# Optimization experiments

Hardware: AMD Instinct MI355X
Metric: run time of the kernel (lower is better)

The kernel has to match this reference:

```python
import jax, jax.numpy as jnp
import numpy as np

K_MASK = -2.3819763e+38
B, T, D, N, K, H = 2, 4096, 2048, 8, 1, 256


def apply_rope(inputs, positions, head_dim):
    # inputs: [B, T, n, H], positions: [B, T]
    fraction = 2.0 * jnp.arange(0, head_dim // 2, dtype=jnp.float32) / head_dim
    timescale = 10000.0 ** fraction  # [H/2]
    sinusoid_inp = positions[..., None].astype(jnp.float32) / timescale  # [B,T,H/2]
    sinusoid_inp = sinusoid_inp[..., None, :]  # [B,T,1,H/2]
    sin, cos = jnp.sin(sinusoid_inp), jnp.cos(sinusoid_inp)
    first_half, second_half = jnp.split(inputs, 2, axis=-1)
    first_part = first_half * cos - second_half * sin
    second_part = second_half * cos + first_half * sin
    return jnp.concatenate([first_part, second_part], axis=-1).astype(inputs.dtype)


def setup_inputs() -> dict:
    key = jax.random.key(0)
    kx, kq, kkv, ko = jax.random.split(key, 4)
    x = jax.random.normal(kx, (B, T, D), dtype=jnp.float32)
    segment_pos = jnp.broadcast_to(jnp.arange(T, dtype=jnp.int32), (B, T))
    attn_mask = jnp.broadcast_to(
        jnp.tril(jnp.ones((T, T), dtype=bool)), (B, T, T))  # causal
    q_w = jax.random.normal(kq, (N, D, H), dtype=jnp.float32) * 0.02
    kv_w = jax.random.normal(kkv, (2, K, D, H), dtype=jnp.float32) * 0.02
    out_w = jax.random.normal(ko, (N, H, D), dtype=jnp.float32) * 0.02
    return {"x": x, "segment_pos": segment_pos, "attn_mask": attn_mask,
            "q_w": q_w, "kv_w": kv_w, "out_w": out_w}


def reference(x, segment_pos, attn_mask, q_w, kv_w, out_w):
    # Projections (GQA branch: num_kv_heads != num_heads)
    query_proj = jnp.einsum('btd,ndh->btnh', x, q_w)          # [B,T,N,H]
    kv_proj = jnp.einsum('bsd,ckdh->cbskh', x, kv_w)          # [2,B,T,K,H]
    key_proj, value_proj = kv_proj[0], kv_proj[1]

    query_proj = apply_rope(query_proj, segment_pos, head_dim=H)
    query_scaled = query_proj * H ** (-0.5)
    key_proj = apply_rope(key_proj, segment_pos, head_dim=H)

    # Repeat KV heads for GQA (num_kv_heads == 1 -> N heads)
    value_proj = jnp.repeat(value_proj, N, axis=-2)           # [B,S,N,H]
    key_proj = jnp.repeat(key_proj, N, axis=-2)               # [B,S,N,H]

    logits = jnp.einsum('btnh,bsnh->btns', query_scaled, key_proj)
    padded_logits = jnp.where(attn_mask[:, :, None, :], logits, K_MASK)
    probs = jax.nn.softmax(padded_logits, axis=-1).astype(key_proj.dtype)
    encoded = jnp.einsum('btns,bsnh->btnh', probs, value_proj)
    attn_output = jnp.einsum('btnh,nhd->btd', encoded, out_w)
    return attn_output
```

## Files before the change

kernel.cpp:

```cpp
#include <hip/hip_runtime.h>

#define T_SEQ 4096
#define D_MODEL 2048
#define N_HEADS 8
#define HDIM 256

typedef unsigned int uint32;
typedef unsigned short u16;
typedef __attribute__((ext_vector_type(8))) short short8;
typedef __attribute__((ext_vector_type(4))) float f32x4;

__device__ __forceinline__ float bf2f(u16 v) {
  return __uint_as_float(((uint32)v) << 16);
}
__device__ __forceinline__ u16 f2bf(float f) {
  uint32 u = __float_as_uint(f);
  u += 0x7fffu + ((u >> 16) & 1u);
  return (u16)(u >> 16);
}
__device__ __forceinline__ uint2 pack4(const f32x4 v) {
  uint2 r;
  r.x = (uint32)f2bf(v[0]) | ((uint32)f2bf(v[1]) << 16);
  r.y = (uint32)f2bf(v[2]) | ((uint32)f2bf(v[3]) << 16);
  return r;
}
__device__ __forceinline__ void gload16(const u16* g, u16* l) {
  __builtin_amdgcn_global_load_lds(
      (const __attribute__((address_space(1))) unsigned int*)g,
      (__attribute__((address_space(3))) unsigned int*)l, 16, 0, 0);
}

__global__ __launch_bounds__(256) void convert_x(const float* __restrict__ x,
                                                 u16* __restrict__ xb) {
  const int idx = blockIdx.x * 256 + threadIdx.x;
  float4 v = *(const float4*)(x + (size_t)idx * 4);
  uint2 pk;
  pk.x = (uint32)f2bf(v.x) | ((uint32)f2bf(v.y) << 16);
  pk.y = (uint32)f2bf(v.z) | ((uint32)f2bf(v.w) << 16);
  *(uint2*)(xb + (size_t)idx * 4) = pk;
}

__global__ __launch_bounds__(256) void prep_weights(
    const float* __restrict__ qw, const float* __restrict__ kvw,
    const float* __restrict__ ow, u16* __restrict__ Wt, u16* __restrict__ Owt) {
  __shared__ float Ts[64][65];
  const int t = threadIdx.x;
  const int tx = blockIdx.x, ty = blockIdx.y, z = blockIdx.z;
  const float* src;
  int srcStride;
  u16* dst;
  if (z == 0) {
    const int c0 = tx * 64;
    const float* base = (c0 < 2048)
                            ? qw + (size_t)(c0 >> 8) * D_MODEL * HDIM
                            : kvw + (size_t)((c0 - 2048) >> 8) * D_MODEL * HDIM;
    src = base + (c0 & 255);
    srcStride = HDIM;
    dst = Wt + (size_t)c0 * D_MODEL;
  } else {
    if (tx >= 32) return;
    src = ow + tx * 64;
    srcStride = D_MODEL;
    dst = Owt + (size_t)tx * 64 * D_MODEL;
  }
  const int d0 = ty * 64;
  const int r = t >> 4, c4 = (t & 15) * 4;
#pragma unroll
  for (int i = 0; i < 4; ++i) {
    float4 v = *(const float4*)(src + (size_t)(d0 + r + i * 16) * srcStride + c4);
    *(float4*)&Ts[r + i * 16][c4] = v;
  }
  __syncthreads();
#pragma unroll
  for (int i = 0; i < 4; ++i) {
    const int crow = r + i * 16;
    uint2 pk;
    pk.x = (uint32)f2bf(Ts[c4 + 0][crow]) | ((uint32)f2bf(Ts[c4 + 1][crow]) << 16);
    pk.y = (uint32)f2bf(Ts[c4 + 2][crow]) | ((uint32)f2bf(Ts[c4 + 3][crow]) << 16);
    *(uint2*)(dst + (size_t)crow * D_MODEL + d0 + c4) = pk;
  }
}

__global__ __launch_bounds__(256) void gemm_qkv_mfma(
    const u16* __restrict__ xb, const u16* __restrict__ Wt,
    u16* __restrict__ Qb, u16* __restrict__ Kb, u16* __restrict__ Vt) {
  __shared__ u16 Asm[128][32];
  __shared__ u16 Bsm[128][32];
  const int t = threadIdx.x;
  const int w = t >> 6, l = t & 63, quad = l >> 4, lq = l & 15;
  const int wm = w & 1, wn = w >> 1;
  const int col0 = blockIdx.x * 128, row0 = blockIdx.y * 128;
  const u16* ga0 = xb + (size_t)(row0 + (t >> 2)) * D_MODEL + (t & 3) * 8;
  const u16* ga1 = ga0 + (size_t)64 * D_MODEL;
  const u16* gb0 = Wt + (size_t)(col0 + (t >> 2)) * D_MODEL + (t & 3) * 8;
  const u16* gb1 = gb0 + (size_t)64 * D_MODEL;
  u16* lA0 = &Asm[0][0] + t * 8;
  u16* lA1 = lA0 + 2048;
  u16* lB0 = &Bsm[0][0] + t * 8;
  u16* lB1 = lB0 + 2048;
  f32x4 acc[4][4];
#pragma unroll
  for (int i = 0; i < 4; ++i)
#pragma unroll
    for (int j = 0; j < 4; ++j) acc[i][j] = (f32x4){0.f, 0.f, 0.f, 0.f};
  for (int k0 = 0; k0 < D_MODEL; k0 += 32) {
    gload16(ga0 + k0, lA0);
    gload16(ga1 + k0, lA1);
    gload16(gb0 + k0, lB0);
    gload16(gb1 + k0, lB1);
    __syncthreads();
    short8 af[4], bf[4];
#pragma unroll
    for (int i = 0; i < 4; ++i)
      af[i] = *(const short8*)&Asm[wm * 64 + i * 16 + lq][quad * 8];
#pragma unroll
    for (int j = 0; j < 4; ++j)
      bf[j] = *(const short8*)&Bsm[wn * 64 + j * 16 + lq][quad * 8];
#pragma unroll
    for (int i = 0; i < 4; ++i)
#pragma unroll
      for (int j = 0; j < 4; ++j)
        acc[i][j] =
            __builtin_amdgcn_mfma_f32_16x16x32_bf16(af[i], bf[j], acc[i][j], 0, 0, 0);
    __syncthreads();
  }
  const int b = row0 >> 12, sbase = row0 & 4095;
#pragma unroll
  for (int i = 0; i < 4; ++i) {
    const int rowloc = wm * 64 + i * 16 + quad * 4;
#pragma unroll
    for (int j = 0; j < 4; ++j) {
      const int col = col0 + wn * 64 + j * 16 + lq;
      if (col < 2048) {
#pragma unroll
        for (int r = 0; r < 4; ++r)
          Qb[(size_t)(row0 + rowloc + r) * 2048 + col] = f2bf(acc[i][j][r]);
      } else if (col < 2304) {
#pragma unroll
        for (int r = 0; r < 4; ++r)
          Kb[(size_t)(row0 + rowloc + r) * HDIM + (col - 2048)] =
              f2bf(acc[i][j][r]);
      } else {
        *(uint2*)(Vt + ((size_t)b * HDIM + col - 2304) * T_SEQ + sbase + rowloc) =
            pack4(acc[i][j]);
      }
    }
  }
}

__global__ __launch_bounds__(256) void rope_kernel(u16* __restrict__ Qb,
                                                   u16* __restrict__ Kb,
                                                   const int* __restrict__ segpos) {
  const int bt = blockIdx.x;
  const int tid = threadIdx.x;
  const float fpos = (float)segpos[bt];
  const float k_ln = 9.210340371976184f / 128.0f;
  for (int p = tid; p < 1024; p += 256) {
    const int n = p >> 7, i = p & 127;
    const size_t base = (size_t)bt * (N_HEADS * HDIM) + (size_t)n * HDIM;
    const float th = fpos * expf(-(float)i * k_ln);
    float s, c;
    sincosf(th, &s, &c);
    const float f1 = bf2f(Qb[base + i]);
    const float f2 = bf2f(Qb[base + i + 128]);
    Qb[base + i] = f2bf((f1 * c - f2 * s) * 0.0625f);
    Qb[base + i + 128] = f2bf((f2 * c + f1 * s) * 0.0625f);
  }
  if (tid < 128) {
    const int i = tid;
    const size_t base = (size_t)bt * HDIM;
    const float th = fpos * expf(-(float)i * k_ln);
    float s, c;
    sincosf(th, &s, &c);
    const float f1 = bf2f(Kb[base + i]);
    const float f2 = bf2f(Kb[base + i + 128]);
    Kb[base + i] = f2bf(f1 * c - f2 * s);
    Kb[base + i + 128] = f2bf(f2 * c + f1 * s);
  }
}

__global__ __launch_bounds__(256) void attn_mfma(const u16* __restrict__ Qb,
                                                 const u16* __restrict__ Kb,
                                                 const u16* __restrict__ Vt,
                                                 u16* __restrict__ Eb) {
  __shared__ u16 Ks[32][264];
  __shared__ u16 Vs[256][40];
  __shared__ u16 Ps[4][16][40];
  const int t = threadIdx.x;
  const int w = t >> 6, l = t & 63;
  const int quad = l >> 4, lq = l & 15;
  const int bid = blockIdx.x;
  const int n = blockIdx.y, b = blockIdx.z;
  const u16* kgbase = Kb + (size_t)b * T_SEQ * HDIM;
  const u16* vgbase = Vt + (size_t)b * HDIM * T_SEQ;

#pragma unroll 1
  for (int ti = 0; ti < 2; ++ti) {
    const int qt = ti ? bid : 63 - bid;
    const int q0 = qt * 64;
    const int wrow0 = q0 + w * 16;

    short8 qf[8];
    {
      const u16* qbase = Qb +
          (((size_t)b * T_SEQ + wrow0 + lq) * N_HEADS + n) * HDIM + quad * 8;
#pragma unroll
      for (int c = 0; c < 8; ++c) qf[c] = *(const short8*)(qbase + c * 32);
    }
    f32x4 O[16];
#pragma unroll
    for (int i = 0; i < 16; ++i) O[i] = (f32x4){0.f, 0.f, 0.f, 0.f};
    float m_i[4] = {-1e30f, -1e30f, -1e30f, -1e30f};
    float l_i[4] = {0.f, 0.f, 0.f, 0.f};

    const int nst = 2 * qt + 2;
    for (int st = 0; st < nst; ++st) {
      const int s0 = st * 32;
      __syncthreads();
#pragma unroll
      for (int p = 0; p < 4; ++p) {
        const int chunk = p * 256 + t;
        const int row = chunk >> 5, col = chunk & 31;
        *(uint4*)&Ks[row][col * 8] =
            *(const uint4*)(kgbase + (size_t)(s0 + row) * HDIM + col * 8);
      }
#pragma unroll
      for (int p = 0; p < 4; ++p) {
        const int chunk = p * 256 + t;
        const int row = chunk >> 2, c4 = chunk & 3;
        *(uint4*)&Vs[row][c4 * 8] =
            *(const uint4*)(vgbase + (size_t)row * T_SEQ + s0 + c4 * 8);
      }
      __syncthreads();
      if (s0 <= wrow0 + 15) {
        f32x4 sa0 = (f32x4){0.f, 0.f, 0.f, 0.f};
        f32x4 sa1 = (f32x4){0.f, 0.f, 0.f, 0.f};
#pragma unroll
        for (int c = 0; c < 8; ++c) {
          short8 k0 = *(const short8*)&Ks[lq][c * 32 + quad * 8];
          short8 k1 = *(const short8*)&Ks[16 + lq][c * 32 + quad * 8];
          sa0 = __builtin_amdgcn_mfma_f32_16x16x32_bf16(qf[c], k0, sa0, 0, 0, 0);
          sa1 = __builtin_amdgcn_mfma_f32_16x16x32_bf16(qf[c], k1, sa1, 0, 0, 0);
        }
        if (s0 + 31 > wrow0) {
#pragma unroll
          for (int r = 0; r < 4; ++r) {
            const int rw = wrow0 + quad * 4 + r;
            if (s0 + lq > rw) sa0[r] = -1e30f;
            if (s0 + 16 + lq > rw) sa1[r] = -1e30f;
          }
        }
        float al[4];
#pragma unroll
        for (int r = 0; r < 4; ++r) {
          float mx = fmaxf(sa0[r], sa1[r]);
          mx = fmaxf(mx, __shfl_xor(mx, 1));
          mx = fmaxf(mx, __shfl_xor(mx, 2));
          mx = fmaxf(mx, __shfl_xor(mx, 4));
          mx = fmaxf(mx, __shfl_xor(mx, 8));
          const float mnew = fmaxf(m_i[r], mx);
          const float a = __expf(m_i[r] - mnew);
          const float p0 = __expf(sa0[r] - mnew);
          const float p1 = __expf(sa1[r] - mnew);
          float rs = p0 + p1;
          rs += __shfl_xor(rs, 1);
          rs += __shfl_xor(rs, 2);
          rs += __shfl_xor(rs, 4);
          rs += __shfl_xor(rs, 8);
          l_i[r] = l_i[r] * a + rs;
          m_i[r] = mnew;
          al[r] = a;
          Ps[w][quad * 4 + r][lq] = f2bf(p0);
          Ps[w][quad * 4 + r][16 + lq] = f2bf(p1);
        }
#pragma unroll
        for (int ntl = 0; ntl < 16; ++ntl) {
          O[ntl][0] *= al[0];
          O[ntl][1] *= al[1];
          O[ntl][2] *= al[2];
          O[ntl][3] *= al[3];
        }
        __asm__ volatile("s_waitcnt lgkmcnt(0)" ::: "memory");
        short8 pf = *(const short8*)&Ps[w][lq][quad * 8];
#pragma unroll
        for (int ntl = 0; ntl < 16; ++ntl) {
          short8 vf = *(const short8*)&Vs[ntl * 16 + lq][quad * 8];
          O[ntl] = __builtin_amdgcn_mfma_f32_16x16x32_bf16(pf, vf, O[ntl], 0, 0, 0);
        }
      }
    }
    float inv[4];
#pragma unroll
    for (int r = 0; r < 4; ++r) inv[r] = 1.0f / l_i[r];
    u16* ebase =
        Eb + (((size_t)b * T_SEQ + wrow0 + quad * 4) * N_HEADS + n) * HDIM + lq;
#pragma unroll
    for (int ntl = 0; ntl < 16; ++ntl)
#pragma unroll
      for (int r = 0; r < 4; ++r)
        ebase[(size_t)r * (N_HEADS * HDIM) + ntl * 16] = f2bf(O[ntl][r] * inv[r]);
  }
}

__global__ __launch_bounds__(256) void gemm_out_mfma(const u16* __restrict__ E,
                                                     const u16* __restrict__ Owt,
                                                     float* __restrict__ out) {
  __shared__ u16 Asm[128][32];
  __shared__ u16 Bsm[128][32];
  const int t = threadIdx.x;
  const int w = t >> 6, l = t & 63, quad = l >> 4, lq = l & 15;
  const int wm = w & 1, wn = w >> 1;
  const int col0 = blockIdx.x * 128, row0 = blockIdx.y * 128;
  const u16* ga0 = E + (size_t)(row0 + (t >> 2)) * D_MODEL + (t & 3) * 8;
  const u16* ga1 = ga0 + (size_t)64 * D_MODEL;
  const u16* gb0 = Owt + (size_t)(col0 + (t >> 2)) * D_MODEL + (t & 3) * 8;
  const u16* gb1 = gb0 + (size_t)64 * D_MODEL;
  u16* lA0 = &Asm[0][0] + t * 8;
  u16* lA1 = lA0 + 2048;
  u16* lB0 = &Bsm[0][0] + t * 8;
  u16* lB1 = lB0 + 2048;
  f32x4 acc[4][4];
#pragma unroll
  for (int i = 0; i < 4; ++i)
#pragma unroll
    for (int j = 0; j < 4; ++j) acc[i][j] = (f32x4){0.f, 0.f, 0.f, 0.f};
  for (int k0 = 0; k0 < D_MODEL; k0 += 32) {
    gload16(ga0 + k0, lA0);
    gload16(ga1 + k0, lA1);
    gload16(gb0 + k0, lB0);
    gload16(gb1 + k0, lB1);
    __syncthreads();
    short8 af[4], bf[4];
#pragma unroll
    for (int i = 0; i < 4; ++i)
      af[i] = *(const short8*)&Asm[wm * 64 + i * 16 + lq][quad * 8];
#pragma unroll
    for (int j = 0; j < 4; ++j)
      bf[j] = *(const short8*)&Bsm[wn * 64 + j * 16 + lq][quad * 8];
#pragma unroll
    for (int i = 0; i < 4; ++i)
#pragma unroll
      for (int j = 0; j < 4; ++j)
        acc[i][j] =
            __builtin_amdgcn_mfma_f32_16x16x32_bf16(af[i], bf[j], acc[i][j], 0, 0, 0);
    __syncthreads();
  }
#pragma unroll
  for (int i = 0; i < 4; ++i) {
    const int row = row0 + wm * 64 + i * 16 + quad * 4;
#pragma unroll
    for (int j = 0; j < 4; ++j) {
      const int col = col0 + wn * 64 + j * 16 + lq;
#pragma unroll
      for (int r = 0; r < 4; ++r)
        out[(size_t)(row + r) * D_MODEL + col] = acc[i][j][r];
    }
  }
}

extern "C" void kernel_launch(void* const* d_in, const int* in_sizes, int n_in,
                              void* d_out, int out_size, void* d_ws,
                              size_t ws_size, hipStream_t stream) {
  const float* x = (const float*)d_in[0];
  const int* segpos = (const int*)d_in[1];
  const float* qw = (const float*)d_in[3];
  const float* kvw = (const float*)d_in[4];
  const float* ow = (const float*)d_in[5];
  float* out = (float*)d_out;

  char* ws = (char*)d_ws;
  u16* Qb = (u16*)ws;
  u16* Kb = (u16*)(ws + (size_t)33554432);
  u16* Vt = (u16*)(ws + (size_t)37748736);
  u16* xb = (u16*)(ws + (size_t)41943040);
  u16* Eb = xb;
  u16* Wt = (u16*)(ws + (size_t)75497472);
  u16* Owt = (u16*)(ws + (size_t)85983232);

  hipLaunchKernelGGL(convert_x, dim3(16384), dim3(256), 0, stream, x, xb);
  hipLaunchKernelGGL(prep_weights, dim3(40, 32, 2), dim3(256), 0, stream, qw,
                     kvw, ow, Wt, Owt);
  hipLaunchKernelGGL(gemm_qkv_mfma, dim3(20, 64), dim3(256), 0, stream, xb, Wt,
                     Qb, Kb, Vt);
  hipLaunchKernelGGL(rope_kernel, dim3(8192), dim3(256), 0, stream, Qb, Kb,
                     segpos);
  hipLaunchKernelGGL(attn_mfma, dim3(32, N_HEADS, 2), dim3(256), 0, stream, Qb,
                     Kb, Vt, Eb);
  hipLaunchKernelGGL(gemm_out_mfma, dim3(16, 64), dim3(256), 0, stream, Eb, Owt,
                     out);
}
```

Before: 815.6 us.

## Double-buffer attention K/V tiles with async LDS loads and in-register P exchange

Rewrites the attention inner loop so K and V tiles are staged into double-buffered LDS through global_load_lds, with the next tile's load overlapping the current tile's MFMA work. K is stored with an XOR swizzle to avoid bank conflicts. The QK^T MFMA operands are swapped so each lane owns one query row. This turns the softmax row reductions into a few cross-quad shuffles and lets the P tile move into MFMA operand layout by register shuffles instead of an LDS round trip. It also adds a lazy rescale that only updates the running max when it grows by more than 8, plus s_setprio hints and an occupancy-2 launch bound. The risks are manual vmcnt bookkeeping, register pressure from the occupancy hint, and a subtle numerics change from the skipped rescale.

```diff
diff --git a/kernel.cpp b/kernel.cpp
--- a/kernel.cpp
+++ b/kernel.cpp
@@ -9,6 +9,7 @@
 typedef unsigned short u16;
 typedef __attribute__((ext_vector_type(8))) short short8;
 typedef __attribute__((ext_vector_type(4))) float f32x4;
+typedef __attribute__((ext_vector_type(4))) uint32 u32x4;
 
 __device__ __forceinline__ float bf2f(u16 v) {
   return __uint_as_float(((uint32)v) << 16);
@@ -17,6 +18,9 @@
   uint32 u = __float_as_uint(f);
   u += 0x7fffu + ((u >> 16) & 1u);
   return (u16)(u >> 16);
+}
+__device__ __forceinline__ uint32 pkbf(float x, float y) {
+  return (uint32)f2bf(x) | ((uint32)f2bf(y) << 16);
 }
 __device__ __forceinline__ uint2 pack4(const f32x4 v) {
   uint2 r;
@@ -179,20 +183,40 @@
   }
 }
 
-__global__ __launch_bounds__(256) void attn_mfma(const u16* __restrict__ Qb,
-                                                 const u16* __restrict__ Kb,
-                                                 const u16* __restrict__ Vt,
-                                                 u16* __restrict__ Eb) {
-  __shared__ u16 Ks[32][264];
-  __shared__ u16 Vs[256][40];
-  __shared__ u16 Ps[4][16][40];
+__global__ __launch_bounds__(256, 2) void attn_mfma(const u16* __restrict__ Qb,
+                                                    const u16* __restrict__ Kb,
+                                                    const u16* __restrict__ Vt,
+                                                    u16* __restrict__ Eb) {
+  __shared__ u16 KsB[2][8192];
+  __shared__ u16 VsB[2][8192];
   const int t = threadIdx.x;
   const int w = t >> 6, l = t & 63;
   const int quad = l >> 4, lq = l & 15;
+  const int sx = lq & 7;
   const int bid = blockIdx.x;
   const int n = blockIdx.y, b = blockIdx.z;
   const u16* kgbase = Kb + (size_t)b * T_SEQ * HDIM;
   const u16* vgbase = Vt + (size_t)b * HDIM * T_SEQ;
+
+  int koff[4], voff[4], ldo[4];
+#pragma unroll
+  for (int p = 0; p < 4; ++p) {
+    const int cid = w * 4 + p;
+    const int krow = 2 * cid + (l >> 5);
+    const int kchk = (l & 31) ^ (krow & 7);
+    koff[p] = krow * HDIM + kchk * 8;
+    voff[p] = (cid * 16 + (l >> 2)) * T_SEQ + (l & 3) * 8;
+    ldo[p] = cid * 512 + l * 8;
+  }
+
+  auto stage = [&](int buf, int s0) {
+#pragma unroll
+    for (int p = 0; p < 4; ++p)
+      gload16(kgbase + (size_t)s0 * HDIM + koff[p], &KsB[buf][ldo[p]]);
+#pragma unroll
+    for (int p = 0; p < 4; ++p)
+      gload16(vgbase + (size_t)voff[p] + s0, &VsB[buf][ldo[p]]);
+  };
 
 #pragma unroll 1
   for (int ti = 0; ti < 2; ++ti) {
@@ -207,98 +231,111 @@
 #pragma unroll
       for (int c = 0; c < 8; ++c) qf[c] = *(const short8*)(qbase + c * 32);
     }
+    stage(0, 0);
+
     f32x4 O[16];
 #pragma unroll
     for (int i = 0; i < 16; ++i) O[i] = (f32x4){0.f, 0.f, 0.f, 0.f};
-    float m_i[4] = {-1e30f, -1e30f, -1e30f, -1e30f};
-    float l_i[4] = {0.f, 0.f, 0.f, 0.f};
+    float m_i = -1e30f, l_i = 0.f;
 
     const int nst = 2 * qt + 2;
+    int cur = 0;
+#pragma unroll 1
     for (int st = 0; st < nst; ++st) {
       const int s0 = st * 32;
-      __syncthreads();
-#pragma unroll
-      for (int p = 0; p < 4; ++p) {
-        const int chunk = p * 256 + t;
-        const int row = chunk >> 5, col = chunk & 31;
-        *(uint4*)&Ks[row][col * 8] =
-            *(const uint4*)(kgbase + (size_t)(s0 + row) * HDIM + col * 8);
+      if (st + 1 < nst) {
+        stage(cur ^ 1, s0 + 32);
+        asm volatile("s_waitcnt vmcnt(8)" ::: "memory");
+      } else {
+        asm volatile("s_waitcnt vmcnt(0)" ::: "memory");
       }
-#pragma unroll
-      for (int p = 0; p < 4; ++p) {
-        const int chunk = p * 256 + t;
-        const int row = chunk >> 2, c4 = chunk & 3;
-        *(uint4*)&Vs[row][c4 * 8] =
-            *(const uint4*)(vgbase + (size_t)row * T_SEQ + s0 + c4 * 8);
-      }
-      __syncthreads();
+      __builtin_amdgcn_s_barrier();
       if (s0 <= wrow0 + 15) {
+        const u16* Kc = &KsB[cur][0];
         f32x4 sa0 = (f32x4){0.f, 0.f, 0.f, 0.f};
         f32x4 sa1 = (f32x4){0.f, 0.f, 0.f, 0.f};
+        __builtin_amdgcn_s_setprio(1);
 #pragma unroll
         for (int c = 0; c < 8; ++c) {
-          short8 k0 = *(const short8*)&Ks[lq][c * 32 + quad * 8];
-          short8 k1 = *(const short8*)&Ks[16 + lq][c * 32 + quad * 8];
-          sa0 = __builtin_amdgcn_mfma_f32_16x16x32_bf16(qf[c], k0, sa0, 0, 0, 0);
-          sa1 = __builtin_amdgcn_mfma_f32_16x16x32_bf16(qf[c], k1, sa1, 0, 0, 0);
+          const int cb = ((c * 4 + quad) ^ sx) * 8;
+          short8 k0 = *(const short8*)&Kc[lq * 256 + cb];
+          short8 k1 = *(const short8*)&Kc[(16 + lq) * 256 + cb];
+          sa0 = __builtin_amdgcn_mfma_f32_16x16x32_bf16(k0, qf[c], sa0, 0, 0, 0);
+          sa1 = __builtin_amdgcn_mfma_f32_16x16x32_bf16(k1, qf[c], sa1, 0, 0, 0);
         }
+        __builtin_amdgcn_s_setprio(0);
         if (s0 + 31 > wrow0) {
+          const int qrow = wrow0 + lq;
 #pragma unroll
           for (int r = 0; r < 4; ++r) {
-            const int rw = wrow0 + quad * 4 + r;
-            if (s0 + lq > rw) sa0[r] = -1e30f;
-            if (s0 + 16 + lq > rw) sa1[r] = -1e30f;
+            if (s0 + quad * 4 + r > qrow) sa0[r] = -1e30f;
+            if (s0 + 16 + quad * 4 + r > qrow) sa1[r] = -1e30f;
           }
         }
-        float al[4];
-#pragma unroll
-        for (int r = 0; r < 4; ++r) {
-          float mx = fmaxf(sa0[r], sa1[r]);
-          mx = fmaxf(mx, __shfl_xor(mx, 1));
-          mx = fmaxf(mx, __shfl_xor(mx, 2));
-          mx = fmaxf(mx, __shfl_xor(mx, 4));
-          mx = fmaxf(mx, __shfl_xor(mx, 8));
-          const float mnew = fmaxf(m_i[r], mx);
-          const float a = __expf(m_i[r] - mnew);
-          const float p0 = __expf(sa0[r] - mnew);
-          const float p1 = __expf(sa1[r] - mnew);
-          float rs = p0 + p1;
-          rs += __shfl_xor(rs, 1);
-          rs += __shfl_xor(rs, 2);
-          rs += __shfl_xor(rs, 4);
-          rs += __shfl_xor(rs, 8);
-          l_i[r] = l_i[r] * a + rs;
-          m_i[r] = mnew;
-          al[r] = a;
-          Ps[w][quad * 4 + r][lq] = f2bf(p0);
-          Ps[w][quad * 4 + r][16 + lq] = f2bf(p1);
+        float mx = fmaxf(fmaxf(fmaxf(sa0[0], sa0[1]), fmaxf(sa0[2], sa0[3])),
+                         fmaxf(fmaxf(sa1[0], sa1[1]), fmaxf(sa1[2], sa1[3])));
+        mx = fmaxf(mx, __shfl_xor(mx, 16));
+        mx = fmaxf(mx, __shfl_xor(mx, 32));
+        if (!__all(mx - m_i <= 8.f)) {
+          const float mnew = fmaxf(m_i, mx);
+          const float a = __expf(m_i - mnew);
+          l_i *= a;
+          m_i = mnew;
+#pragma unroll
+          for (int r = 0; r < 4; ++r) {
+            const float ar = __shfl(a, quad * 4 + r);
+#pragma unroll
+            for (int ntl = 0; ntl < 16; ++ntl) O[ntl][r] *= ar;
+          }
         }
+        const float p0 = __expf(sa0[0] - m_i), p1 = __expf(sa0[1] - m_i);
+        const float p2 = __expf(sa0[2] - m_i), p3 = __expf(sa0[3] - m_i);
+        const float p4 = __expf(sa1[0] - m_i), p5 = __expf(sa1[1] - m_i);
+        const float p6 = __expf(sa1[2] - m_i), p7 = __expf(sa1[3] - m_i);
+        float rs = ((p0 + p1) + (p2 + p3)) + ((p4 + p5) + (p6 + p7));
+        rs += __shfl_xor(rs, 16);
+        rs += __shfl_xor(rs, 32);
+        l_i += rs;
+        const uint32 a0 = pkbf(p0, p1), a1 = pkbf(p2, p3);
+        const uint32 b0 = pkbf(p4, p5), b1 = pkbf(p6, p7);
+        const uint32 s10 = (quad < 2) ? b0 : a0;
+        const uint32 s11 = (quad < 2) ? b1 : a1;
+        const uint32 r10 = __shfl_xor(s10, 32);
+        const uint32 r11 = __shfl_xor(s11, 32);
+        const bool sR = (quad == 0) || (quad == 3);
+        const uint32 s20 = sR ? r10 : ((quad == 1) ? a0 : b0);
+        const uint32 s21 = sR ? r11 : ((quad == 1) ? a1 : b1);
+        const uint32 r20 = __shfl_xor(s20, 16);
+        const uint32 r21 = __shfl_xor(s21, 16);
+        const uint32 w0 = (quad == 0) ? a0 : (quad == 2) ? r10 : r20;
+        const uint32 w1 = (quad == 0) ? a1 : (quad == 2) ? r11 : r21;
+        const uint32 w2 = (quad == 1) ? r10 : (quad == 3) ? b0 : r20;
+        const uint32 w3 = (quad == 1) ? r11 : (quad == 3) ? b1 : r21;
+        const u32x4 pw = (u32x4){w0, w1, w2, w3};
+        const short8 pf = __builtin_bit_cast(short8, pw);
+        const u16* Vc = &VsB[cur][lq * 32 + quad * 8];
+        __builtin_amdgcn_s_setprio(1);
 #pragma unroll
         for (int ntl = 0; ntl < 16; ++ntl) {
-          O[ntl][0] *= al[0];
-          O[ntl][1] *= al[1];
-          O[ntl][2] *= al[2];
-          O[ntl][3] *= al[3];
-        }
-        __asm__ volatile("s_waitcnt lgkmcnt(0)" ::: "memory");
-        short8 pf = *(const short8*)&Ps[w][lq][quad * 8];
-#pragma unroll
-        for (int ntl = 0; ntl < 16; ++ntl) {
-          short8 vf = *(const short8*)&Vs[ntl * 16 + lq][quad * 8];
+          short8 vf = *(const short8*)&Vc[ntl * 512];
           O[ntl] = __builtin_amdgcn_mfma_f32_16x16x32_bf16(pf, vf, O[ntl], 0, 0, 0);
         }
+        __builtin_amdgcn_s_setprio(0);
       }
+      __builtin_amdgcn_s_barrier();
+      cur ^= 1;
     }
-    float inv[4];
-#pragma unroll
-    for (int r = 0; r < 4; ++r) inv[r] = 1.0f / l_i[r];
+    const float inv = 1.0f / l_i;
+    float invq[4];
+#pragma unroll
+    for (int r = 0; r < 4; ++r) invq[r] = __shfl(inv, quad * 4 + r);
     u16* ebase =
         Eb + (((size_t)b * T_SEQ + wrow0 + quad * 4) * N_HEADS + n) * HDIM + lq;
 #pragma unroll
     for (int ntl = 0; ntl < 16; ++ntl)
 #pragma unroll
       for (int r = 0; r < 4; ++r)
-        ebase[(size_t)r * (N_HEADS * HDIM) + ntl * 16] = f2bf(O[ntl][r] * inv[r]);
+        ebase[(size_t)r * (N_HEADS * HDIM) + ntl * 16] = f2bf(O[ntl][r] * invq[r]);
   }
 }
 
```

Result: faster. 703.8 us (-13.7%).
